# Optimization experiments

Hardware: AMD Instinct MI355X
Metric: run time of the kernel (lower is better)

## Reference

```python
import jax, jax.numpy as jnp
import numpy as np

N = 50000      # nodes
E = 800000     # edges
D = 128        # input feature dim
H = 8          # heads
U = 32         # units per head (model width = H*U = 256)
L = 2          # attention layers
OUT = 64       # output dim


def setup_inputs() -> dict:
    key = jax.random.key(0)
    ks = jax.random.split(key, 8)
    node_states = jax.random.normal(ks[0], (N, D), jnp.float32)
    edges = jax.random.randint(ks[1], (E, 2), 0, N, jnp.int32)
    s = 0.05  # small init scale keeps pre-clip scores in a sane range
    W_pre = jax.random.normal(ks[2], (D, H * U), jnp.float32) * s
    b_pre = jnp.zeros((H * U,), jnp.float32)
    W_att = jax.random.normal(ks[3], (L, H, H * U, U), jnp.float32) * s
    a_att = jax.random.normal(ks[4], (L, H, 2 * U), jnp.float32) * s
    W_out = jax.random.normal(ks[5], (H * U, OUT), jnp.float32) * s
    b_out = jnp.zeros((OUT,), jnp.float32)
    return {"node_states": node_states, "edges": edges, "W_pre": W_pre,
            "b_pre": b_pre, "W_att": W_att, "a_att": a_att,
            "W_out": W_out, "b_out": b_out}


def _gat_multihead(x, src, dst, W, a):
    """One MultiHeadGraphAttention layer. x:[N,HU], W:[H,HU,U], a:[H,2U].
    Returns relu(concat over heads):[N,HU]."""
    n = x.shape[0]
    h = jnp.einsum('nd,hdu->hnu', x, W)                     # [H,N,U]
    # concat([h_src, h_dst]) @ a  ==  a_src.h_src + a_dst.h_dst
    s_src = jnp.einsum('hnu,hu->hn', h, a[:, :U])           # [H,N]
    s_dst = jnp.einsum('hnu,hu->hn', h, a[:, U:])           # [H,N]
    e = jax.nn.leaky_relu(s_src[:, src] + s_dst[:, dst], negative_slope=0.2)
    e = jnp.exp(jnp.clip(e, -2.0, 2.0))                     # [H,E]
    den = jax.vmap(lambda v: jax.ops.segment_sum(v, src, num_segments=n))(e)
    alpha = e / den[:, src]                                 # [H,E]
    msgs = h[:, dst, :] * alpha[..., None]                  # [H,E,U]
    agg = jax.vmap(lambda m: jax.ops.segment_sum(m, src, num_segments=n))(msgs)
    return jax.nn.relu(agg.transpose(1, 0, 2).reshape(n, -1))  # [N,HU]


def reference(node_states, edges, W_pre, b_pre, W_att, a_att, W_out, b_out):
    src, dst = edges[:, 0], edges[:, 1]
    x = jax.nn.relu(node_states @ W_pre + b_pre)            # [N,HU]
    for l in range(L):
        x = _gat_multihead(x, src, dst, W_att[l], a_att[l]) + x
    return x @ W_out + b_out                                # [N,OUT]
```

## Files before the change

### kernel.cpp

```cpp
#include <hip/hip_runtime.h>
#include <hip/hip_bf16.h>
#include <hip/hip_fp8.h>

#define N_NODES 50000
#define E_EDGES 800000
#define D_IN    128
#define HU      256
#define H_HEADS 8
#define U_DIM   32
#define OUT_DIM 64
#define CAP     64
#define H_SCALE 32.0f
#define DEGS    16

typedef __attribute__((ext_vector_type(8))) short short8v;
typedef __attribute__((ext_vector_type(4))) float f32x4;
typedef unsigned short u16;
typedef unsigned char u8;
typedef __attribute__((ext_vector_type(4))) unsigned short u16x4;
typedef __attribute__((ext_vector_type(8))) unsigned short u16x8;

__device__ __forceinline__ float bf2f(u16 v) {
    return __uint_as_float(((unsigned)v) << 16);
}
__device__ __forceinline__ u16 f2b(float f) {
    unsigned u = __float_as_uint(f);
    return (u16)((u + 0x7FFFu + ((u >> 16) & 1u)) >> 16);
}
__device__ __forceinline__ u8 f2fp8(float f) {
    __hip_fp8_e4m3 t(f);
    return (u8)t.__x;
}

__global__ __launch_bounds__(256) void adj_fill(const int* __restrict__ edges,
                                                int* __restrict__ deg,
                                                u16* __restrict__ adj) {
    int tid = blockIdx.x * 256 + threadIdx.x;
    if (tid >= E_EDGES / 4) return;
    const int4* E4 = (const int4*)edges;
    int4 p0 = E4[tid * 2];
    int4 p1 = E4[tid * 2 + 1];
    int sx[4] = {p0.x, p0.z, p1.x, p1.z};
    int dx[4] = {p0.y, p0.w, p1.y, p1.w};
    int slot[4];
#pragma unroll
    for (int i = 0; i < 4; ++i)
        slot[i] = atomicAdd(&deg[sx[i] * DEGS], 1);
#pragma unroll
    for (int i = 0; i < 4; ++i)
        if (slot[i] < CAP) adj[(size_t)sx[i] * CAP + slot[i]] = (u16)dx[i];
}

template<int K, int N, bool GAT>
__device__ __forceinline__ void wfrag_one(const float* __restrict__ W,
                                          u16* __restrict__ Wf, int tid) {
    int j  = tid & 7;
    int l  = (tid >> 3) & 63;
    int fb = tid >> 9;
    int ks = fb % (K / 32);
    int ct = fb / (K / 32);
    int k  = ks * 32 + (l >> 4) * 8 + j;
    int n  = ct * 16 + (l & 15);
    float v = GAT ? W[(size_t)(n >> 5) * (K * 32) + k * 32 + (n & 31)]
                  : W[(size_t)k * N + n];
    Wf[tid] = f2b(v);
}

__device__ __forceinline__ void wa_one(const float* __restrict__ Watt,
                                       const float* __restrict__ al,
                                       u16* __restrict__ Wfs, int tid) {
    int j  = tid & 7;
    int l  = (tid >> 3) & 63;
    int ks = tid >> 9;
    int k  = ks * 32 + (l >> 4) * 8 + j;
    int n  = l & 15;
    int hd = n & 7;
    int off = (n < 8) ? 0 : 32;
    float s = 0.f;
#pragma unroll
    for (int u = 0; u < 32; ++u)
        s += Watt[(size_t)hd * 8192 + k * 32 + u] * al[hd * 64 + off + u];
    Wfs[tid] = f2b(s);
}

__global__ __launch_bounds__(256) void wfrag_all(const float* __restrict__ Wpre,
                                                 const float* __restrict__ Watt,
                                                 const float* __restrict__ aatt,
                                                 const float* __restrict__ Wout,
                                                 u16* __restrict__ wf_pre,
                                                 u16* __restrict__ wf_a0,
                                                 u16* __restrict__ wf_a1,
                                                 u16* __restrict__ wf_out,
                                                 u16* __restrict__ wfs0,
                                                 u16* __restrict__ wfs1,
                                                 int* __restrict__ deg) {
    int tid = blockIdx.x * 256 + threadIdx.x;
    for (int i = tid; i < (N_NODES * DEGS) / 4; i += 736 * 256)
        ((int4*)deg)[i] = make_int4(0, 0, 0, 0);
    if (tid < 32768)        wfrag_one<D_IN, HU, false>(Wpre, wf_pre, tid);
    else if (tid < 98304)   wfrag_one<HU, HU, true>(Watt, wf_a0, tid - 32768);
    else if (tid < 163840)  wfrag_one<HU, HU, true>(Watt + 65536, wf_a1, tid - 98304);
    else if (tid < 180224)  wfrag_one<HU, OUT_DIM, false>(Wout, wf_out, tid - 163840);
    else if (tid < 184320)  wa_one(Watt, aatt, wfs0, tid - 180224);
    else if (tid < 188416)  wa_one(Watt + 65536, aatt + 512, wfs1, tid - 184320);
}

template<int K, int N, int MT, int NT, int MODE, bool ABF16>
__global__ __launch_bounds__(256) void mfma_gemm(const void* __restrict__ Ain,
                                                 const u16* __restrict__ Wf,
                                                 const float* __restrict__ bias,
                                                 void* __restrict__ Cout,
                                                 const u16* __restrict__ wfs,
                                                 u16* __restrict__ sb,
                                                 u16* __restrict__ db) {
    constexpr int SK = K + 8;
    __shared__ __align__(16) u16 as[64 * SK];
    int t  = threadIdx.x;
    int n0 = blockIdx.x * 64;

    if (ABF16) {
        constexpr int K8 = K / 8;
        const u16x8* A8 = (const u16x8*)Ain;
        for (int i = t; i < 64 * K8; i += 256) {
            int row = i / K8, c8 = i % K8;
            u16x8 v = {0, 0, 0, 0, 0, 0, 0, 0};
            if (n0 + row < N_NODES)
                v = __builtin_nontemporal_load(&A8[(size_t)(n0 + row) * K8 + c8]);
            *(u16x8*)&as[row * SK + c8 * 8] = v;
        }
    } else {
        constexpr int K4 = K / 4;
        const f32x4* A4 = (const f32x4*)Ain;
        for (int i = t; i < 64 * K4; i += 256) {
            int row = i / K4, c4 = i % K4;
            f32x4 v = {0.f, 0.f, 0.f, 0.f};
            if (n0 + row < N_NODES)
                v = __builtin_nontemporal_load(&A4[(size_t)(n0 + row) * K4 + c4]);
            u16x4 pk;
            pk.x = f2b(v.x); pk.y = f2b(v.y); pk.z = f2b(v.z); pk.w = f2b(v.w);
            *(u16x4*)&as[row * SK + c4 * 4] = pk;
        }
    }
    __syncthreads();

    int wid = t >> 6, l = t & 63;
    constexpr int NWN = N / (NT * 16);
    int col0 = (wid % NWN) * (NT * 16);
    int row0 = (wid / NWN) * (MT * 16);

    f32x4 acc[MT][NT];
#pragma unroll
    for (int mt = 0; mt < MT; ++mt)
#pragma unroll
        for (int nt = 0; nt < NT; ++nt)
            acc[mt][nt] = (f32x4){0.f, 0.f, 0.f, 0.f};
    f32x4 accs[MT];
#pragma unroll
    for (int mt = 0; mt < MT; ++mt) accs[mt] = (f32x4){0.f, 0.f, 0.f, 0.f};

    int ar  = l & 15;
    int akb = (l >> 4) * 8;
#pragma unroll
    for (int ks = 0; ks < K / 32; ++ks) {
        short8v a[MT], b[NT];
#pragma unroll
        for (int mt = 0; mt < MT; ++mt)
            a[mt] = *(const short8v*)&as[(row0 + mt * 16 + ar) * SK + ks * 32 + akb];
#pragma unroll
        for (int nt = 0; nt < NT; ++nt)
            b[nt] = *(const short8v*)&Wf[(size_t)(((((col0 >> 4) + nt) * (K / 32)) + ks) * 64 + l) * 8];
        if (MODE == 1) {
            if (wid == 0) {
                short8v bs = *(const short8v*)&wfs[(size_t)(ks * 64 + l) * 8];
#pragma unroll
                for (int mt = 0; mt < MT; ++mt)
                    accs[mt] = __builtin_amdgcn_mfma_f32_16x16x32_bf16(a[mt], bs, accs[mt], 0, 0, 0);
            }
        }
#pragma unroll
        for (int mt = 0; mt < MT; ++mt)
#pragma unroll
            for (int nt = 0; nt < NT; ++nt)
                acc[mt][nt] = __builtin_amdgcn_mfma_f32_16x16x32_bf16(a[mt], b[nt], acc[mt][nt], 0, 0, 0);
    }

    int crow = (l >> 4) * 4, ccol = l & 15;
#pragma unroll
    for (int mt = 0; mt < MT; ++mt) {
#pragma unroll
        for (int nt = 0; nt < NT; ++nt) {
            int gc = col0 + nt * 16 + ccol;
#pragma unroll
            for (int r = 0; r < 4; ++r) {
                int gr = n0 + row0 + mt * 16 + crow + r;
                if (gr >= N_NODES) continue;
                float v = acc[mt][nt][r];
                if (MODE == 0) {
                    v += bias[gc];
                    ((u16*)Cout)[(size_t)gr * N + gc] = f2b(fmaxf(v, 0.f));
                } else if (MODE == 1) {
                    ((u8*)Cout)[(size_t)gr * N + gc] = f2fp8(v * H_SCALE);
                } else {
                    ((float*)Cout)[(size_t)gr * N + gc] = v + bias[gc];
                }
            }
        }
    }
    if (MODE == 1) {
        if (wid == 0) {
#pragma unroll
            for (int mt = 0; mt < MT; ++mt) {
#pragma unroll
                for (int r = 0; r < 4; ++r) {
                    int gr = n0 + mt * 16 + crow + r;
                    if (gr >= N_NODES) continue;
                    float v = accs[mt][r];
                    if (ccol < 8) sb[(size_t)gr * 8 + ccol] = f2b(v);
                    else          db[(size_t)gr * 8 + ccol - 8] = f2b(v);
                }
            }
        }
    }
}

__global__ __launch_bounds__(256) void agg_kernel(const u8* __restrict__ hb,
                                                  const u16* __restrict__ ssrcb,
                                                  const u16* __restrict__ sdstb,
                                                  const int* __restrict__ deg,
                                                  const u16* __restrict__ adj,
                                                  u16* __restrict__ x) {
    __shared__ u16 sd_lds[4][64 * 8];
    int t  = threadIdx.x & 63;
    int wv = threadIdx.x >> 6;
    int n  = blockIdx.x * 4 + wv;
    int dg = deg[(size_t)n * DEGS];
    dg = dg > CAP ? CAP : dg;
    int dl = (t < dg) ? (int)__builtin_nontemporal_load(&adj[(size_t)n * CAP + t]) : 0;
    u16x8 sdrow = *(const u16x8*)(sdstb + (size_t)dl * 8);
    *(u16x8*)&sd_lds[wv][t * 8] = sdrow;
    __syncthreads();

    int hd8 = t & 7;
    float ss_s = bf2f(ssrcb[(size_t)n * 8 + hd8]);
    int q   = t >> 4;
    int sub = t & 15;
    int hdg = sub >> 1;

    float a[16];
#pragma unroll
    for (int i = 0; i < 16; ++i) a[i] = 0.f;
    float den_part = 0.f;

    if (dg <= 32) {
        int nq = (dg + 3) >> 2;
        uint4 hv0, hv1, hv2, hv3, hv4, hv5, hv6, hv7;
        {
            uint4* hvp[8] = {&hv0, &hv1, &hv2, &hv3, &hv4, &hv5, &hv6, &hv7};
#pragma unroll
            for (int i = 0; i < 8; ++i) {
                if (i < nq) {
                    int d = __shfl(dl, i * 4 + q);
                    *hvp[i] = *(const uint4*)(hb + (size_t)d * HU + sub * 16);
                }
            }
        }
        float w[4];
#pragma unroll
        for (int sg = 0; sg < 4; ++sg) {
            int eidx = sg * 8 + (t >> 3);
            float ww = 0.f;
            if (eidx < dg) {
                float sc = ss_s + bf2f(sd_lds[wv][eidx * 8 + hd8]);
                sc = sc > 0.f ? sc : 0.2f * sc;
                sc = fminf(fmaxf(sc, -2.f), 2.f);
                ww = __expf(sc);
            }
            w[sg] = ww;
            den_part += ww;
        }
        const uint4* hvp[8] = {&hv0, &hv1, &hv2, &hv3, &hv4, &hv5, &hv6, &hv7};
#pragma unroll
        for (int i = 0; i < 8; ++i) {
            if (i < nq) {
                int e4 = i * 4 + q;
                float we = __shfl(w[i >> 1], ((e4 & 7) << 3) | hdg);
                if (e4 < dg) {
                    uint4 hvv = *hvp[i];
#pragma unroll
                    for (int k = 0; k < 4; ++k) {
                        unsigned dw = (&hvv.x)[k];
                        auto lo = __builtin_amdgcn_cvt_pk_f32_fp8(dw, false);
                        auto hi = __builtin_amdgcn_cvt_pk_f32_fp8(dw, true);
                        a[4 * k + 0] += we * lo[0];
                        a[4 * k + 1] += we * lo[1];
                        a[4 * k + 2] += we * hi[0];
                        a[4 * k + 3] += we * hi[1];
                    }
                }
            }
        }
    } else {
        for (int base = 0; base < dg; base += 8) {
            int eidx = base + (t >> 3);
            float w = 0.f;
            if (eidx < dg) {
                float sc = ss_s + bf2f(sd_lds[wv][eidx * 8 + hd8]);
                sc = sc > 0.f ? sc : 0.2f * sc;
                sc = fminf(fmaxf(sc, -2.f), 2.f);
                w = __expf(sc);
            }
            den_part += w;
#pragma unroll
            for (int g = 0; g < 2; ++g) {
                int e4 = base + g * 4 + q;
                int d  = __shfl(dl, e4);
                float we = __shfl(w, ((g * 4 + q) << 3) | hdg);
                if (e4 < dg) {
                    uint4 hvv = *(const uint4*)(hb + (size_t)d * HU + sub * 16);
#pragma unroll
                    for (int k = 0; k < 4; ++k) {
                        unsigned dw = (&hvv.x)[k];
                        auto lo = __builtin_amdgcn_cvt_pk_f32_fp8(dw, false);
                        auto hi = __builtin_amdgcn_cvt_pk_f32_fp8(dw, true);
                        a[4 * k + 0] += we * lo[0];
                        a[4 * k + 1] += we * lo[1];
                        a[4 * k + 2] += we * hi[0];
                        a[4 * k + 3] += we * hi[1];
                    }
                }
            }
        }
    }

    den_part += __shfl_xor(den_part, 8);
    den_part += __shfl_xor(den_part, 16);
    den_part += __shfl_xor(den_part, 32);
#pragma unroll
    for (int i = 0; i < 16; ++i) {
        a[i] += __shfl_xor(a[i], 16);
        a[i] += __shfl_xor(a[i], 32);
    }

    if (q == 0) {
        float den = __shfl(den_part, hdg);
        float inv = dg > 0 ? (1.f / den) * (1.f / H_SCALE) : 0.f;
        size_t xo = (size_t)n * HU + sub * 16;
        u16x8 xv0 = __builtin_nontemporal_load((const u16x8*)(x + xo));
        u16x8 xv1 = __builtin_nontemporal_load((const u16x8*)(x + xo + 8));
        u16x8 o0, o1;
#pragma unroll
        for (int i = 0; i < 8; ++i) {
            o0[i] = f2b(fmaxf(a[i] * inv, 0.f) + bf2f((u16)xv0[i]));
            o1[i] = f2b(fmaxf(a[8 + i] * inv, 0.f) + bf2f((u16)xv1[i]));
        }
        __builtin_nontemporal_store(o0, (u16x8*)(x + xo));
        __builtin_nontemporal_store(o1, (u16x8*)(x + xo + 8));
    }
}

extern "C" void kernel_launch(void* const* d_in, const int* in_sizes, int n_in,
                              void* d_out, int out_size, void* d_ws, size_t ws_size,
                              hipStream_t stream) {
    const float* ns   = (const float*)d_in[0];
    const int*   edges= (const int*)d_in[1];
    const float* Wpre = (const float*)d_in[2];
    const float* bpre = (const float*)d_in[3];
    const float* Watt = (const float*)d_in[4];
    const float* aatt = (const float*)d_in[5];
    const float* Wout = (const float*)d_in[6];
    const float* bout = (const float*)d_in[7];
    float* out = (float*)d_out;

    char* p = (char*)d_ws;
    u16* xA = (u16*)p;               p += (size_t)N_NODES * HU * 2;
    u8* h = (u8*)p;                  p += (size_t)N_NODES * HU;
    u16* ssrcb = (u16*)p;            p += (size_t)N_NODES * H_HEADS * 2;
    u16* sdstb = (u16*)p;            p += (size_t)N_NODES * H_HEADS * 2;
    int* deg = (int*)p;              p += (size_t)N_NODES * DEGS * 4;
    u16* adj = (u16*)p;              p += (size_t)N_NODES * CAP * 2;
    u16* wf_pre  = (u16*)p;          p += (size_t)D_IN * HU * 2;
    u16* wf_att0 = (u16*)p;          p += (size_t)HU * HU * 2;
    u16* wf_att1 = (u16*)p;          p += (size_t)HU * HU * 2;
    u16* wf_out  = (u16*)p;          p += (size_t)HU * OUT_DIM * 2;
    u16* wfs0 = (u16*)p;             p += (size_t)4096 * 2;
    u16* wfs1 = (u16*)p;             p += (size_t)4096 * 2;

    wfrag_all<<<736, 256, 0, stream>>>(Wpre, Watt, aatt, Wout,
                                       wf_pre, wf_att0, wf_att1, wf_out, wfs0, wfs1, deg);

    adj_fill<<<(E_EDGES / 4 + 255) / 256, 256, 0, stream>>>(edges, deg, adj);

    const int GB = (N_NODES + 63) / 64;
    mfma_gemm<D_IN, HU, 4, 4, 0, false><<<GB, 256, 0, stream>>>(
        ns, wf_pre, bpre, xA, nullptr, nullptr, nullptr);

    u16* wf_att[2] = {wf_att0, wf_att1};
    u16* wfs[2] = {wfs0, wfs1};
    for (int l = 0; l < 2; ++l) {
        mfma_gemm<HU, HU, 4, 4, 1, true><<<GB, 256, 0, stream>>>(
            xA, wf_att[l], nullptr, h, wfs[l], ssrcb, sdstb);
        agg_kernel<<<(N_NODES / 4), 256, 0, stream>>>(h, ssrcb, sdstb, deg, adj, xA);
    }

    mfma_gemm<HU, OUT_DIM, 1, 4, 2, true><<<GB, 256, 0, stream>>>(
        xA, wf_out, bout, out, nullptr, nullptr, nullptr);
}
```

Baseline: 239.4 us.

## Partition adjacency fill by source-node range across block groups

Reworks adj_fill so each of 8 block groups handles only edges whose source falls in its node range, and every group scans the whole edge list. The aim is to keep the atomics and adjacency writes of each group in a smaller region of deg/adj, which may map onto a single XCD's L2 if blockIdx is assigned round-robin across XCDs, and so cut cross-die atomic contention. The cost is reading the edge list eight times and running fewer blocks, each with a serial strided loop.

```diff
diff --git a/kernel.cpp b/kernel.cpp
--- a/kernel.cpp
+++ b/kernel.cpp
@@ -12,6 +12,9 @@
 #define CAP     64
 #define H_SCALE 32.0f
 #define DEGS    16
+#define NPART   8
+#define PART_N  (N_NODES / NPART)
+#define ADJ_BPP 96
 
 typedef __attribute__((ext_vector_type(8))) short short8v;
 typedef __attribute__((ext_vector_type(4))) float f32x4;
@@ -35,20 +38,25 @@
 __global__ __launch_bounds__(256) void adj_fill(const int* __restrict__ edges,
                                                 int* __restrict__ deg,
                                                 u16* __restrict__ adj) {
-    int tid = blockIdx.x * 256 + threadIdx.x;
-    if (tid >= E_EDGES / 4) return;
+    int pt = blockIdx.x & (NPART - 1);
+    int bi = blockIdx.x >> 3;
+    int lo = pt * PART_N, hi = lo + PART_N;
     const int4* E4 = (const int4*)edges;
-    int4 p0 = E4[tid * 2];
-    int4 p1 = E4[tid * 2 + 1];
-    int sx[4] = {p0.x, p0.z, p1.x, p1.z};
-    int dx[4] = {p0.y, p0.w, p1.y, p1.w};
-    int slot[4];
-#pragma unroll
-    for (int i = 0; i < 4; ++i)
-        slot[i] = atomicAdd(&deg[sx[i] * DEGS], 1);
-#pragma unroll
-    for (int i = 0; i < 4; ++i)
-        if (slot[i] < CAP) adj[(size_t)sx[i] * CAP + slot[i]] = (u16)dx[i];
+    const int TOT4 = E_EDGES / 2;
+    const int chunk = (TOT4 + ADJ_BPP - 1) / ADJ_BPP;
+    int s = bi * chunk;
+    int e = s + chunk; if (e > TOT4) e = TOT4;
+    for (int i = s + (int)threadIdx.x; i < e; i += 256) {
+        int4 p = E4[i];
+        if (p.x >= lo && p.x < hi) {
+            int sl = atomicAdd(&deg[p.x * DEGS], 1);
+            if (sl < CAP) adj[(size_t)p.x * CAP + sl] = (u16)p.y;
+        }
+        if (p.z >= lo && p.z < hi) {
+            int sl = atomicAdd(&deg[p.z * DEGS], 1);
+            if (sl < CAP) adj[(size_t)p.z * CAP + sl] = (u16)p.w;
+        }
+    }
 }
 
 template<int K, int N, bool GAT>
@@ -388,7 +396,7 @@
     wfrag_all<<<736, 256, 0, stream>>>(Wpre, Watt, aatt, Wout,
                                        wf_pre, wf_att0, wf_att1, wf_out, wfs0, wfs1, deg);
 
-    adj_fill<<<(E_EDGES / 4 + 255) / 256, 256, 0, stream>>>(edges, deg, adj);
+    adj_fill<<<NPART * ADJ_BPP, 256, 0, stream>>>(edges, deg, adj);
 
     const int GB = (N_NODES + 63) / 64;
     mfma_gemm<D_IN, HU, 4, 4, 0, false><<<GB, 256, 0, stream>>>(
```

New measurement: 224.6 us, median of 2. 6.2% less time.
